# Optimization experiments

Hardware: AMD Instinct MI355X
Metric: run time of the kernel (lower is better)

The kernel has to match this reference:

```python
import jax, jax.numpy as jnp
import numpy as np

B, SEQ, DIM, D, K = 32, 2048, 512, 512, 128


def _ln(x, g, b, eps=1e-5):
    m = x.mean(-1, keepdims=True)
    v = ((x - m) ** 2).mean(-1, keepdims=True)
    return (x - m) / jnp.sqrt(v + eps) * g + b


def _gelu(v):
    return jax.nn.gelu(v, approximate=False)


def _diff_topk(s, k, t):
    # s: (B, N) scores; iterative relaxed top-k (Xie & Ermon style).
    def step(carry, _):
        a = jax.nn.softmax(carry / t, axis=-1)
        carry = carry + jnp.log(jnp.clip(1.0 - a, 1e-6, 1.0))
        return carry, a
    _, Ws = jax.lax.scan(step, s, None, length=k)  # (k, B, N)
    return jnp.transpose(Ws, (1, 0, 2))            # (B, k, N)


def setup_inputs():
    key = jax.random.key(0)
    ks = jax.random.split(key, 6)
    w = lambda k_, shape: jax.random.normal(k_, shape, dtype=jnp.float32) * 0.02
    return {
        'x': jax.random.normal(ks[0], (B, SEQ, DIM), dtype=jnp.float32),
        'tau': jnp.array(0.0, dtype=jnp.float32),
        'ln1_g': jnp.ones((DIM,), jnp.float32), 'ln1_b': jnp.zeros((DIM,), jnp.float32),
        'W1': w(ks[1], (DIM, D)), 'b1': jnp.zeros((D,), jnp.float32),
        'ln2_g': jnp.ones((SEQ,), jnp.float32), 'ln2_b': jnp.zeros((SEQ,), jnp.float32),
        'W2': w(ks[2], (SEQ, SEQ)), 'b2': jnp.zeros((SEQ,), jnp.float32),
        'ln3_g': jnp.ones((D,), jnp.float32), 'ln3_b': jnp.zeros((D,), jnp.float32),
        'W3': w(ks[3], (D, D + 1)), 'b3': jnp.zeros((D + 1,), jnp.float32),
        'ln4_g': jnp.ones((D,), jnp.float32), 'ln4_b': jnp.zeros((D,), jnp.float32),
        'W4': w(ks[4], (D, DIM)), 'b4': jnp.zeros((DIM,), jnp.float32),
    }


def reference(x, tau, ln1_g, ln1_b, W1, b1, ln2_g, ln2_b, W2, b2,
              ln3_g, ln3_b, W3, b3, ln4_g, ln4_b, W4, b4):
    # tok_proj: LN(dim) -> Linear(dim, D) -> GELU
    x_tok = _gelu(_ln(x, ln1_g, ln1_b) @ W1 + b1)                  # (B, N, D)
    # ch_proj over the token axis: LN(seq) -> Linear(seq, seq) -> GELU
    xt = jnp.swapaxes(x_tok, 1, 2)                                  # (B, D, N)
    x_ch = jnp.swapaxes(_gelu(_ln(xt, ln2_g, ln2_b) @ W2 + b2), 1, 2)
    # proj -> split score | features
    h = _ln(x_tok + x_ch, ln3_g, ln3_b) @ W3 + b3                   # (B, N, D+1)
    x_score, x_proj = h[..., 0], h[..., 1:]
    t = jax.nn.sigmoid(jnp.clip(tau, -2.0, 5.0))
    Wmat = _diff_topk(x_score, K, t)                                # (B, k, N)
    Z = jnp.einsum('bkn,bnd->bkd', Wmat, x_proj)                    # soft gather
    Y = jnp.einsum('bkn,bkd->bnd', Wmat, Z)                         # soft scatter
    return _ln(x_proj + Y, ln4_g, ln4_b) @ W4 + b4                  # (B, N, dim)
```

## Files before the change

kernel.cpp:

```cpp
#include <hip/hip_runtime.h>
#include <math.h>

#define B_   32
#define SEQ_ 2048
#define DIM_ 512
#define KSEL 128

typedef _Float16 f16;
typedef _Float16 half8 __attribute__((ext_vector_type(8)));
typedef float floatx4 __attribute__((ext_vector_type(4)));

#define LSTR2 32

__device__ __forceinline__ float gelu_exact(float v) {
  return 0.5f * v * (1.0f + erff(v * 0.70710678118654752440f));
}

__global__ __launch_bounds__(256) void rowstats512(const float* __restrict__ X,
                                                   float* __restrict__ mean,
                                                   float* __restrict__ rstd) {
  int row = blockIdx.x * 4 + (threadIdx.x >> 6);
  int l = threadIdx.x & 63;
  const float4* p = (const float4*)(X + (size_t)row * 512);
  float4 v0 = p[l * 2], v1 = p[l * 2 + 1];
  float s = v0.x + v0.y + v0.z + v0.w + v1.x + v1.y + v1.z + v1.w;
  float q = v0.x*v0.x + v0.y*v0.y + v0.z*v0.z + v0.w*v0.w
          + v1.x*v1.x + v1.y*v1.y + v1.z*v1.z + v1.w*v1.w;
#pragma unroll
  for (int off = 32; off > 0; off >>= 1) {
    s += __shfl_down(s, off);
    q += __shfl_down(q, off);
  }
  if (l == 0) {
    float m = s * (1.0f / 512.0f);
    float var = q * (1.0f / 512.0f) - m * m;
    mean[row] = m;
    rstd[row] = rsqrtf(var + 1e-5f);
  }
}

__global__ __launch_bounds__(256) void rowstats512_f16(const f16* __restrict__ X,
                                                       float* __restrict__ mean,
                                                       float* __restrict__ rstd) {
  int row = blockIdx.x * 4 + (threadIdx.x >> 6);
  int l = threadIdx.x & 63;
  half8 h = *(const half8*)(X + (size_t)row * 512 + l * 8);
  float s = 0.f, q = 0.f;
#pragma unroll
  for (int i = 0; i < 8; ++i) { float v = (float)h[i]; s += v; q += v * v; }
#pragma unroll
  for (int off = 32; off > 0; off >>= 1) {
    s += __shfl_down(s, off);
    q += __shfl_down(q, off);
  }
  if (l == 0) {
    float m = s * (1.0f / 512.0f);
    float var = q * (1.0f / 512.0f) - m * m;
    mean[row] = m;
    rstd[row] = rsqrtf(var + 1e-5f);
  }
}

__global__ __launch_bounds__(512) void colstats_part(const f16* __restrict__ xtok,
                                                     float2* __restrict__ part) {
  int b = blockIdx.x >> 3, pr = blockIdx.x & 7;
  int d = threadIdx.x;
  const f16* src = xtok + ((size_t)b * SEQ_ + (size_t)pr * 256) * 512 + d;
  float s = 0.f, q = 0.f;
#pragma unroll 4
  for (int i = 0; i < 256; ++i) {
    float v = (float)src[(size_t)i * 512];
    s += v; q += v * v;
  }
  part[(size_t)blockIdx.x * 512 + d] = make_float2(s, q);
}

__global__ __launch_bounds__(256) void colstats_fin(const float2* __restrict__ part,
                                                    float* __restrict__ mean,
                                                    float* __restrict__ rstd) {
  int idx = blockIdx.x * 256 + threadIdx.x;
  int b = idx >> 9;
  float s = 0.f, q = 0.f;
#pragma unroll
  for (int p = 0; p < 8; ++p) {
    float2 v = part[((size_t)(b * 8 + p)) * 512 + (idx & 511)];
    s += v.x; q += v.y;
  }
  float m = s * (1.0f / 2048.0f);
  mean[idx] = m;
  rstd[idx] = rsqrtf(q * (1.0f / 2048.0f) - m * m + 1e-5f);
}

template <typename T>
__global__ __launch_bounds__(256) void transpose_cvt(const T* __restrict__ src,
                                                     f16* __restrict__ dst,
                                                     int R, int C, long sb, long db) {
  __shared__ float tile[32][33];
  const T* s = src + (long)blockIdx.z * sb;
  f16* d = dst + (long)blockIdx.z * db;
  int c0 = blockIdx.x * 32, r0 = blockIdx.y * 32;
  int tx = threadIdx.x, ty = threadIdx.y;
#pragma unroll
  for (int i = 0; i < 4; ++i) {
    int r = r0 + ty + i * 8, c = c0 + tx;
    if (r < R && c < C) tile[ty + i * 8][tx] = (float)s[(long)r * C + c];
  }
  __syncthreads();
#pragma unroll
  for (int i = 0; i < 4; ++i) {
    int c = c0 + ty + i * 8, r = r0 + tx;
    if (c < C && r < R) d[(long)c * R + r] = (f16)tile[tx][ty + i * 8];
  }
}

__global__ __launch_bounds__(256) void trans2_kernel(const f16* __restrict__ xtok,
    const float* __restrict__ mean2, const float* __restrict__ rstd2,
    const float* __restrict__ g2, const float* __restrict__ bl2,
    f16* __restrict__ A2) {
  __shared__ float tile[32][33];
  int b = blockIdx.z;
  const f16* src = xtok + (long)b * SEQ_ * 512;
  f16* dst = A2 + (long)b * 512 * SEQ_;
  int d0 = blockIdx.x * 32, s0 = blockIdx.y * 32;
  int tx = threadIdx.x, ty = threadIdx.y;
  float m = mean2[b * 512 + d0 + tx];
  float rs = rstd2[b * 512 + d0 + tx];
#pragma unroll
  for (int i = 0; i < 4; ++i) {
    int s = s0 + ty + i * 8;
    float v = (float)src[(long)s * 512 + d0 + tx];
    tile[ty + i * 8][tx] = (v - m) * rs * g2[s] + bl2[s];
  }
  __syncthreads();
#pragma unroll
  for (int i = 0; i < 4; ++i) {
    int d = d0 + ty + i * 8, s = s0 + tx;
    dst[(long)d * SEQ_ + s] = (f16)tile[tx][ty + i * 8];
  }
}


__device__ __forceinline__ void stage_gll(const f16* __restrict__ src, long ld,
                                          int row0, int k0, f16* S, int t) {
  int w = t >> 6, lane = t & 63;
  int r = lane >> 2, c8 = (lane & 3) * 8;
#pragma unroll
  for (int i = 0; i < 2; ++i) {
    int chunk = w * 2 + i;
    const f16* g = src + (long)(row0 + chunk * 16 + r) * ld + k0 + c8;
    f16* l = S + chunk * 16 * LSTR2;
    __builtin_amdgcn_global_load_lds(
        (const __attribute__((address_space(1))) void*)g,
        (__attribute__((address_space(3))) void*)l, 16, 0, 0);
  }
}

__device__ __forceinline__ void stage_a_ln_f32(const float* __restrict__ src, long ld,
    const float* __restrict__ mean, const float* __restrict__ rstd,
    const float* __restrict__ g, const float* __restrict__ bl,
    int row0, int k0, f16* S, int t) {
  int row = t >> 1, kc = (t & 1) * 16;
  int r = row0 + row, c = k0 + kc;
  float m = mean[r], sd = rstd[r];
  const float* p = src + (long)r * ld + c;
  float v[16], gv[16], bv[16];
#pragma unroll
  for (int i = 0; i < 4; ++i) {
    float4 q = ((const float4*)p)[i];
    v[i*4+0]=q.x; v[i*4+1]=q.y; v[i*4+2]=q.z; v[i*4+3]=q.w;
    float4 gq = ((const float4*)(g + c))[i];
    gv[i*4+0]=gq.x; gv[i*4+1]=gq.y; gv[i*4+2]=gq.z; gv[i*4+3]=gq.w;
    float4 bq = ((const float4*)(bl + c))[i];
    bv[i*4+0]=bq.x; bv[i*4+1]=bq.y; bv[i*4+2]=bq.z; bv[i*4+3]=bq.w;
  }
  half8 o0, o1;
#pragma unroll
  for (int i = 0; i < 8; ++i) {
    o0[i] = (f16)((v[i] - m) * sd * gv[i] + bv[i]);
    o1[i] = (f16)((v[i + 8] - m) * sd * gv[i + 8] + bv[i + 8]);
  }
  *(half8*)(S + row * LSTR2 + kc) = o0;
  *(half8*)(S + row * LSTR2 + kc + 8) = o1;
}

__device__ __forceinline__ void stage_a_ln_f16(const f16* __restrict__ src, long ld,
    const float* __restrict__ mean, const float* __restrict__ rstd,
    const float* __restrict__ g, const float* __restrict__ bl,
    int row0, int k0, f16* S, int t) {
  int row = t >> 1, kc = (t & 1) * 16;
  int r = row0 + row, c = k0 + kc;
  float m = mean[r], sd = rstd[r];
  const f16* p = src + (long)r * ld + c;
  half8 h0 = *(const half8*)(p);
  half8 h1 = *(const half8*)(p + 8);
  float gv[16], bv[16];
#pragma unroll
  for (int i = 0; i < 4; ++i) {
    float4 gq = ((const float4*)(g + c))[i];
    gv[i*4+0]=gq.x; gv[i*4+1]=gq.y; gv[i*4+2]=gq.z; gv[i*4+3]=gq.w;
    float4 bq = ((const float4*)(bl + c))[i];
    bv[i*4+0]=bq.x; bv[i*4+1]=bq.y; bv[i*4+2]=bq.z; bv[i*4+3]=bq.w;
  }
  half8 o0, o1;
#pragma unroll
  for (int i = 0; i < 8; ++i) {
    o0[i] = (f16)(((float)h0[i] - m) * sd * gv[i] + bv[i]);
    o1[i] = (f16)(((float)h1[i] - m) * sd * gv[i + 8] + bv[i + 8]);
  }
  *(half8*)(S + row * LSTR2 + kc) = o0;
  *(half8*)(S + row * LSTR2 + kc + 8) = o1;
}

__device__ __forceinline__ void mfma_step(const f16* As, const f16* Bs, int lane,
                                          int wr, int wc, floatx4 acc[4][4]) {
  int kc = (lane >> 4) * 8;
  int rl = lane & 15;
  half8 a[4], b[4];
#pragma unroll
  for (int mi = 0; mi < 4; ++mi)
    a[mi] = *(const half8*)(As + (wr * 64 + mi * 16 + rl) * LSTR2 + kc);
#pragma unroll
  for (int ni = 0; ni < 4; ++ni)
    b[ni] = *(const half8*)(Bs + (wc * 64 + ni * 16 + rl) * LSTR2 + kc);
#pragma unroll
  for (int mi = 0; mi < 4; ++mi)
#pragma unroll
    for (int ni = 0; ni < 4; ++ni)
      acc[mi][ni] = __builtin_amdgcn_mfma_f32_16x16x32_f16(a[mi], b[ni], acc[mi][ni], 0, 0, 0);
}

#define GEMM_PROLOG \
  __shared__ __attribute__((aligned(16))) f16 As[128 * LSTR2]; \
  __shared__ __attribute__((aligned(16))) f16 Bs[128 * LSTR2]; \
  int t = threadIdx.x; \
  int lane = t & 63, w = t >> 6, wr = w >> 1, wc = w & 1; \
  floatx4 acc[4][4]; \
  _Pragma("unroll") for (int mi = 0; mi < 4; ++mi) \
  _Pragma("unroll") for (int ni = 0; ni < 4; ++ni) acc[mi][ni] = (floatx4){0.f,0.f,0.f,0.f};

__global__ __launch_bounds__(256) void g1_kernel(const float* __restrict__ x,
    const float* __restrict__ mean, const float* __restrict__ rstd,
    const float* __restrict__ g1, const float* __restrict__ bl1,
    const f16* __restrict__ W1T, const float* __restrict__ b1,
    f16* __restrict__ xtok) {
  GEMM_PROLOG
  int m0 = blockIdx.y * 128, n0 = blockIdx.x * 128;
  for (int k0 = 0; k0 < 512; k0 += 32) {
    stage_a_ln_f32(x, 512, mean, rstd, g1, bl1, m0, k0, As, t);
    stage_gll(W1T, 512, n0, k0, Bs, t);
    __syncthreads();
    mfma_step(As, Bs, lane, wr, wc, acc);
    __syncthreads();
  }
#pragma unroll
  for (int mi = 0; mi < 4; ++mi)
#pragma unroll
    for (int ni = 0; ni < 4; ++ni) {
      int c = n0 + wc * 64 + ni * 16 + (lane & 15);
      float bias = b1[c];
      int r0 = m0 + wr * 64 + mi * 16 + (lane >> 4) * 4;
#pragma unroll
      for (int j = 0; j < 4; ++j)
        xtok[(long)(r0 + j) * 512 + c] = (f16)gelu_exact(acc[mi][ni][j] + bias);
    }
}

__global__ __launch_bounds__(256) void g2_kernel(const f16* __restrict__ W2T,
    const f16* __restrict__ A2, const float* __restrict__ b2,
    const f16* __restrict__ xtok, f16* __restrict__ xsum) {
  GEMM_PROLOG
  int b = blockIdx.z;
  int m0 = blockIdx.y * 128, n0 = blockIdx.x * 128;
  const f16* A2b = A2 + (long)b * 512 * SEQ_;
  const f16* xtb = xtok + (long)b * SEQ_ * 512;
  f16* xsb = xsum + (long)b * SEQ_ * 512;
  for (int k0 = 0; k0 < SEQ_; k0 += 32) {
    stage_gll(W2T, SEQ_, m0, k0, As, t);
    stage_gll(A2b, SEQ_, n0, k0, Bs, t);
    __syncthreads();
    mfma_step(As, Bs, lane, wr, wc, acc);
    __syncthreads();
  }
#pragma unroll
  for (int mi = 0; mi < 4; ++mi)
#pragma unroll
    for (int ni = 0; ni < 4; ++ni) {
      int c = n0 + wc * 64 + ni * 16 + (lane & 15);
      int r0 = m0 + wr * 64 + mi * 16 + (lane >> 4) * 4;
#pragma unroll
      for (int j = 0; j < 4; ++j) {
        int r = r0 + j;
        long idx = (long)r * 512 + c;
        float v = gelu_exact(acc[mi][ni][j] + b2[r]);
        xsb[idx] = (f16)((float)xtb[idx] + v);
      }
    }
}

__global__ __launch_bounds__(256) void g3_kernel(const f16* __restrict__ xsum,
    const float* __restrict__ mean, const float* __restrict__ rstd,
    const float* __restrict__ g3, const float* __restrict__ bl3,
    const f16* __restrict__ BT , const float* __restrict__ b3,
    f16* __restrict__ xproj) {
  GEMM_PROLOG
  int m0 = blockIdx.y * 128, n0 = blockIdx.x * 128;
  for (int k0 = 0; k0 < 512; k0 += 32) {
    stage_a_ln_f16(xsum, 512, mean, rstd, g3, bl3, m0, k0, As, t);
    stage_gll(BT, 512, n0, k0, Bs, t);
    __syncthreads();
    mfma_step(As, Bs, lane, wr, wc, acc);
    __syncthreads();
  }
#pragma unroll
  for (int mi = 0; mi < 4; ++mi)
#pragma unroll
    for (int ni = 0; ni < 4; ++ni) {
      int c = n0 + wc * 64 + ni * 16 + (lane & 15);
      float bias = b3[c + 1];
      int r0 = m0 + wr * 64 + mi * 16 + (lane >> 4) * 4;
#pragma unroll
      for (int j = 0; j < 4; ++j)
        xproj[(long)(r0 + j) * 512 + c] = (f16)(acc[mi][ni][j] + bias);
    }
}

__global__ __launch_bounds__(256) void score_kernel(const f16* __restrict__ xsum,
    const float* __restrict__ mean, const float* __restrict__ rstd,
    const float* __restrict__ g3, const float* __restrict__ bl3,
    const f16* __restrict__ w3c , const float* __restrict__ b3,
    float* __restrict__ xscore) {
  int row = blockIdx.x * 4 + (threadIdx.x >> 6);
  int l = threadIdx.x & 63;
  float m = mean[row], sd = rstd[row];
  half8 h = *(const half8*)(xsum + (long)row * 512 + l * 8);
  half8 wv = *(const half8*)(w3c + l * 8);
  float acc = 0.f;
#pragma unroll
  for (int i = 0; i < 8; ++i) {
    int d = l * 8 + i;
    float v = ((float)h[i] - m) * sd * g3[d] + bl3[d];
    acc += v * (float)wv[i];
  }
#pragma unroll
  for (int off = 32; off > 0; off >>= 1) acc += __shfl_down(acc, off);
  if (l == 0) xscore[row] = acc + b3[0];
}

__global__ __launch_bounds__(256) void topk_kernel(const float* __restrict__ xscore,
                                                   const float* __restrict__ tau,
                                                   f16* __restrict__ Wm) {
  int b = blockIdx.x, t = threadIdx.x;
  __shared__ float red[4];
  float tv = fminf(fmaxf(tau[0], -2.0f), 5.0f);
  float temp = 1.0f / (1.0f + expf(-tv));
  float it = 1.0f / temp;
  float c[8];
  const float* xs = xscore + (size_t)b * SEQ_;
#pragma unroll
  for (int i = 0; i < 8; ++i) c[i] = xs[t * 8 + i];
  for (int k = 0; k < KSEL; ++k) {
    float e[8];
    float p = 0.f;
#pragma unroll
    for (int i = 0; i < 8; ++i) { e[i] = expf(c[i] * it); p += e[i]; }
#pragma unroll
    for (int off = 32; off > 0; off >>= 1) p += __shfl_down(p, off);
    if ((t & 63) == 0) red[t >> 6] = p;
    __syncthreads();
    float S = red[0] + red[1] + red[2] + red[3];
    float iS = 1.0f / S;
    float a[8];
    half8 h;
#pragma unroll
    for (int i = 0; i < 8; ++i) { a[i] = e[i] * iS; h[i] = (f16)a[i]; }
    *(half8*)(Wm + ((size_t)b * KSEL + k) * SEQ_ + t * 8) = h;
#pragma unroll
    for (int i = 0; i < 8; ++i) c[i] += logf(fmaxf(1.0f - a[i], 1e-6f));
    __syncthreads();
  }
}

__global__ __launch_bounds__(256) void gz_kernel(const f16* __restrict__ Wm,
    const f16* __restrict__ xprojT, float* __restrict__ Zpart) {
  GEMM_PROLOG
  int b = blockIdx.z, kc = blockIdx.y;
  int n0 = blockIdx.x * 128;
  const f16* A = Wm + (long)b * KSEL * SEQ_;
  const f16* BT = xprojT + (long)b * 512 * SEQ_;
  float* Zb = Zpart + ((long)b * 2 + kc) * KSEL * 512;
  int kbeg = kc * 1024, kend = kbeg + 1024;
  for (int k0 = kbeg; k0 < kend; k0 += 32) {
    stage_gll(A, SEQ_, 0, k0, As, t);
    stage_gll(BT, SEQ_, n0, k0, Bs, t);
    __syncthreads();
    mfma_step(As, Bs, lane, wr, wc, acc);
    __syncthreads();
  }
#pragma unroll
  for (int mi = 0; mi < 4; ++mi)
#pragma unroll
    for (int ni = 0; ni < 4; ++ni) {
      int c = n0 + wc * 64 + ni * 16 + (lane & 15);
      int r0 = wr * 64 + mi * 16 + (lane >> 4) * 4;
#pragma unroll
      for (int j = 0; j < 4; ++j)
        Zb[(long)(r0 + j) * 512 + c] = acc[mi][ni][j];
    }
}

__global__ __launch_bounds__(256) void ztrans_kernel(const float* __restrict__ Zpart,
                                                     f16* __restrict__ ZT) {
  __shared__ float tile[32][33];
  int b = blockIdx.z;
  int c0 = blockIdx.x * 32, r0 = blockIdx.y * 32;
  int tx = threadIdx.x, ty = threadIdx.y;
  const float* p0 = Zpart + ((long)b * 2 + 0) * KSEL * 512;
  const float* p1 = Zpart + ((long)b * 2 + 1) * KSEL * 512;
#pragma unroll
  for (int i = 0; i < 4; ++i) {
    int r = r0 + ty + i * 8, c = c0 + tx;
    tile[ty + i * 8][tx] = p0[(long)r * 512 + c] + p1[(long)r * 512 + c];
  }
  __syncthreads();
  f16* d = ZT + (long)b * 512 * KSEL;
#pragma unroll
  for (int i = 0; i < 4; ++i) {
    int c = c0 + ty + i * 8, r = r0 + tx;
    d[(long)c * KSEL + r] = (f16)tile[tx][ty + i * 8];
  }
}

__global__ __launch_bounds__(256) void gy_kernel(const f16* __restrict__ WmT,
    const f16* __restrict__ ZT, const f16* __restrict__ xproj,
    f16* __restrict__ rbuf) {
  GEMM_PROLOG
  int b = blockIdx.z;
  int m0 = blockIdx.y * 128, n0 = blockIdx.x * 128;
  const f16* A = WmT + (long)b * SEQ_ * KSEL;
  const f16* BT = ZT + (long)b * 512 * KSEL;
  const f16* xpb = xproj + (long)b * SEQ_ * 512;
  f16* rb = rbuf + (long)b * SEQ_ * 512;
  for (int k0 = 0; k0 < KSEL; k0 += 32) {
    stage_gll(A, KSEL, m0, k0, As, t);
    stage_gll(BT, KSEL, n0, k0, Bs, t);
    __syncthreads();
    mfma_step(As, Bs, lane, wr, wc, acc);
    __syncthreads();
  }
#pragma unroll
  for (int mi = 0; mi < 4; ++mi)
#pragma unroll
    for (int ni = 0; ni < 4; ++ni) {
      int c = n0 + wc * 64 + ni * 16 + (lane & 15);
      int r0 = m0 + wr * 64 + mi * 16 + (lane >> 4) * 4;
#pragma unroll
      for (int j = 0; j < 4; ++j) {
        long idx = (long)(r0 + j) * 512 + c;
        rb[idx] = (f16)((float)xpb[idx] + acc[mi][ni][j]);
      }
    }
}

__global__ __launch_bounds__(256) void g4_kernel(const f16* __restrict__ rbuf,
    const float* __restrict__ mean, const float* __restrict__ rstd,
    const float* __restrict__ g4, const float* __restrict__ bl4,
    const f16* __restrict__ W4T, const float* __restrict__ b4,
    float* __restrict__ out) {
  GEMM_PROLOG
  int m0 = blockIdx.y * 128, n0 = blockIdx.x * 128;
  for (int k0 = 0; k0 < 512; k0 += 32) {
    stage_a_ln_f16(rbuf, 512, mean, rstd, g4, bl4, m0, k0, As, t);
    stage_gll(W4T, 512, n0, k0, Bs, t);
    __syncthreads();
    mfma_step(As, Bs, lane, wr, wc, acc);
    __syncthreads();
  }
#pragma unroll
  for (int mi = 0; mi < 4; ++mi)
#pragma unroll
    for (int ni = 0; ni < 4; ++ni) {
      int c = n0 + wc * 64 + ni * 16 + (lane & 15);
      float bias = b4[c];
      int r0 = m0 + wr * 64 + mi * 16 + (lane >> 4) * 4;
#pragma unroll
      for (int j = 0; j < 4; ++j)
        out[(long)(r0 + j) * 512 + c] = acc[mi][ni][j] + bias;
    }
}

extern "C" void kernel_launch(void* const* d_in, const int* in_sizes, int n_in,
                              void* d_out, int out_size, void* d_ws, size_t ws_size,
                              hipStream_t stream) {
  const float* x    = (const float*)d_in[0];
  const float* tau  = (const float*)d_in[1];
  const float* g1   = (const float*)d_in[2];
  const float* bl1  = (const float*)d_in[3];
  const float* W1   = (const float*)d_in[4];
  const float* b1   = (const float*)d_in[5];
  const float* g2   = (const float*)d_in[6];
  const float* bl2  = (const float*)d_in[7];
  const float* W2   = (const float*)d_in[8];
  const float* b2   = (const float*)d_in[9];
  const float* g3   = (const float*)d_in[10];
  const float* bl3  = (const float*)d_in[11];
  const float* W3   = (const float*)d_in[12];
  const float* b3   = (const float*)d_in[13];
  const float* g4   = (const float*)d_in[14];
  const float* bl4  = (const float*)d_in[15];
  const float* W4   = (const float*)d_in[16];
  const float* b4   = (const float*)d_in[17];
  float* out = (float*)d_out;

  const long NTOK = (long)B_ * SEQ_;

  char* ws = (char*)d_ws;
  f16* regA   = (f16*)(ws);
  f16* regB   = (f16*)(ws + (64l << 20));
  float* Zpart = (float*)(ws + (128l << 20));
  f16* W2T    = (f16*)(ws + (144l << 20));
  f16* W1T    = (f16*)(ws + (152l << 20));
  f16* W3T    = (f16*)(ws + (153l << 20));
  f16* W4T    = (f16*)(ws + (154l << 20));
  float* xscore = (float*)(ws + (155l << 20));
  float* meanA  = (float*)(ws + (156l << 20));
  float* rstdA  = meanA + NTOK;
  float* mean2  = rstdA + NTOK;
  float* rstd2  = mean2 + B_ * 512;
  float2* part  = (float2*)(rstd2 + B_ * 512);

  f16* xtok   = (f16*)d_out;
  f16* xprojT = (f16*)d_out;
  f16* Wm     = (f16*)((char*)d_out + (64l << 20));
  f16* WmT    = (f16*)((char*)d_out + (80l << 20));
  f16* ZT     = (f16*)((char*)d_out + (96l << 20));

  f16* A2    = regA;
  f16* xsum  = regB;
  f16* xproj = regA;
  f16* rbuf  = regB;

  dim3 tb(32, 8);

  transpose_cvt<float><<<dim3(16, 16, 1), tb, 0, stream>>>(W1, W1T, 512, 512, 0, 0);
  transpose_cvt<float><<<dim3(64, 64, 1), tb, 0, stream>>>(W2, W2T, 2048, 2048, 0, 0);
  transpose_cvt<float><<<dim3(17, 16, 1), tb, 0, stream>>>(W3, W3T, 512, 513, 0, 0);
  transpose_cvt<float><<<dim3(16, 16, 1), tb, 0, stream>>>(W4, W4T, 512, 512, 0, 0);

  rowstats512<<<NTOK / 4, 256, 0, stream>>>(x, meanA, rstdA);
  g1_kernel<<<dim3(4, 512), 256, 0, stream>>>(x, meanA, rstdA, g1, bl1, W1T, b1, xtok);

  colstats_part<<<B_ * 8, 512, 0, stream>>>(xtok, part);
  colstats_fin<<<64, 256, 0, stream>>>(part, mean2, rstd2);
  trans2_kernel<<<dim3(16, 64, B_), tb, 0, stream>>>(xtok, mean2, rstd2, g2, bl2, A2);
  g2_kernel<<<dim3(4, 16, B_), 256, 0, stream>>>(W2T, A2, b2, xtok, xsum);

  rowstats512_f16<<<NTOK / 4, 256, 0, stream>>>(xsum, meanA, rstdA);
  score_kernel<<<NTOK / 4, 256, 0, stream>>>(xsum, meanA, rstdA, g3, bl3, W3T, b3, xscore);
  g3_kernel<<<dim3(4, 512), 256, 0, stream>>>(xsum, meanA, rstdA, g3, bl3, W3T + 512, b3, xproj);

  topk_kernel<<<B_, 256, 0, stream>>>(xscore, tau, Wm);

  transpose_cvt<f16><<<dim3(16, 64, B_), tb, 0, stream>>>(xproj, xprojT, 2048, 512,
      (long)SEQ_ * 512, (long)512 * SEQ_);
  transpose_cvt<f16><<<dim3(64, 4, B_), tb, 0, stream>>>(Wm, WmT, 128, 2048,
      (long)KSEL * SEQ_, (long)SEQ_ * KSEL);

  gz_kernel<<<dim3(4, 2, B_), 256, 0, stream>>>(Wm, xprojT, Zpart);
  ztrans_kernel<<<dim3(16, 4, B_), tb, 0, stream>>>(Zpart, ZT);

  gy_kernel<<<dim3(4, 16, B_), 256, 0, stream>>>(WmT, ZT, xproj, rbuf);

  rowstats512_f16<<<NTOK / 4, 256, 0, stream>>>(rbuf, meanA, rstdA);
  g4_kernel<<<dim3(4, 512), 256, 0, stream>>>(rbuf, meanA, rstdA, g4, bl4, W4T, b4, out);
}
```

Measured before the change: 878.3 us.

## Double-buffer GEMMs with 64-wide swizzled K tiles, fuse xproj transpose, widen topk

All MFMA GEMM kernels now stage 64-wide K tiles into double-buffered, XOR-swizzled LDS. The next tile is prefetched while the current one is computed, with one barrier per step and s_setprio raised around the MFMAs. The aim is to overlap global loads with compute and to cut LDS bank conflicts. g3 also writes a transposed copy of xproj directly, which removes a separate transpose pass. topk runs with 512 threads and one barrier per iteration using ping-pong reduction slots. The larger LDS footprint may lower occupancy.

```diff
diff --git a/kernel.cpp b/kernel.cpp
--- a/kernel.cpp
+++ b/kernel.cpp
@@ -8,9 +8,8 @@
 
 typedef _Float16 f16;
 typedef _Float16 half8 __attribute__((ext_vector_type(8)));
+typedef _Float16 half4 __attribute__((ext_vector_type(4)));
 typedef float floatx4 __attribute__((ext_vector_type(4)));
-
-#define LSTR2 32
 
 __device__ __forceinline__ float gelu_exact(float v) {
   return 0.5f * v * (1.0f + erff(v * 0.70710678118654752440f));
@@ -140,100 +139,123 @@
 }
 
 
-__device__ __forceinline__ void stage_gll(const f16* __restrict__ src, long ld,
-                                          int row0, int k0, f16* S, int t) {
-  int w = t >> 6, lane = t & 63;
-  int r = lane >> 2, c8 = (lane & 3) * 8;
-#pragma unroll
-  for (int i = 0; i < 2; ++i) {
-    int chunk = w * 2 + i;
-    const f16* g = src + (long)(row0 + chunk * 16 + r) * ld + k0 + c8;
-    f16* l = S + chunk * 16 * LSTR2;
-    __builtin_amdgcn_global_load_lds(
-        (const __attribute__((address_space(1))) void*)g,
-        (__attribute__((address_space(3))) void*)l, 16, 0, 0);
-  }
-}
-
-__device__ __forceinline__ void stage_a_ln_f32(const float* __restrict__ src, long ld,
+__device__ __forceinline__ void stage_tile_gll(const f16* __restrict__ src, long ld,
+                                               int k0, f16* D0, f16* D1, int t) {
+  int w = t >> 6;
+#pragma unroll
+  for (int kk = 0; kk < 2; ++kk) {
+    f16* dst = kk ? D1 : D0;
+#pragma unroll
+    for (int s = 0; s < 2; ++s) {
+      int row = s * 64 + (t >> 2);
+      int slot = (t & 3) ^ ((row >> 1) & 3);
+      const f16* g = src + (long)row * ld + k0 + kk * 32 + slot * 8;
+      f16* lp = dst + (long)(s * 64 + w * 16) * 32;
+      __builtin_amdgcn_global_load_lds(
+          (const __attribute__((address_space(1))) void*)g,
+          (__attribute__((address_space(3))) void*)lp, 16, 0, 0);
+    }
+  }
+}
+
+__device__ __forceinline__ void stage_a_ln_f32_64(const float* __restrict__ src, long ld,
     const float* __restrict__ mean, const float* __restrict__ rstd,
     const float* __restrict__ g, const float* __restrict__ bl,
-    int row0, int k0, f16* S, int t) {
-  int row = t >> 1, kc = (t & 1) * 16;
-  int r = row0 + row, c = k0 + kc;
+    int row0, int k0, f16* D0, f16* D1, int t) {
+  int row = t >> 1, kk = t & 1;
+  int r = row0 + row;
   float m = mean[r], sd = rstd[r];
-  const float* p = src + (long)r * ld + c;
-  float v[16], gv[16], bv[16];
-#pragma unroll
-  for (int i = 0; i < 4; ++i) {
-    float4 q = ((const float4*)p)[i];
-    v[i*4+0]=q.x; v[i*4+1]=q.y; v[i*4+2]=q.z; v[i*4+3]=q.w;
-    float4 gq = ((const float4*)(g + c))[i];
-    gv[i*4+0]=gq.x; gv[i*4+1]=gq.y; gv[i*4+2]=gq.z; gv[i*4+3]=gq.w;
-    float4 bq = ((const float4*)(bl + c))[i];
-    bv[i*4+0]=bq.x; bv[i*4+1]=bq.y; bv[i*4+2]=bq.z; bv[i*4+3]=bq.w;
-  }
-  half8 o0, o1;
-#pragma unroll
-  for (int i = 0; i < 8; ++i) {
-    o0[i] = (f16)((v[i] - m) * sd * gv[i] + bv[i]);
-    o1[i] = (f16)((v[i + 8] - m) * sd * gv[i + 8] + bv[i + 8]);
-  }
-  *(half8*)(S + row * LSTR2 + kc) = o0;
-  *(half8*)(S + row * LSTR2 + kc + 8) = o1;
-}
-
-__device__ __forceinline__ void stage_a_ln_f16(const f16* __restrict__ src, long ld,
+  f16* dst = (kk ? D1 : D0) + row * 32;
+  int swz = (row >> 1) & 3;
+  const float* p = src + (long)r * ld + k0 + kk * 32;
+  const float* gp = g + k0 + kk * 32;
+  const float* bp = bl + k0 + kk * 32;
+#pragma unroll
+  for (int j = 0; j < 4; ++j) {
+    float4 q0 = *(const float4*)(p + j * 8);
+    float4 q1 = *(const float4*)(p + j * 8 + 4);
+    float4 g0 = *(const float4*)(gp + j * 8);
+    float4 g1 = *(const float4*)(gp + j * 8 + 4);
+    float4 b0 = *(const float4*)(bp + j * 8);
+    float4 b1 = *(const float4*)(bp + j * 8 + 4);
+    half8 o;
+    o[0] = (f16)((q0.x - m) * sd * g0.x + b0.x);
+    o[1] = (f16)((q0.y - m) * sd * g0.y + b0.y);
+    o[2] = (f16)((q0.z - m) * sd * g0.z + b0.z);
+    o[3] = (f16)((q0.w - m) * sd * g0.w + b0.w);
+    o[4] = (f16)((q1.x - m) * sd * g1.x + b1.x);
+    o[5] = (f16)((q1.y - m) * sd * g1.y + b1.y);
+    o[6] = (f16)((q1.z - m) * sd * g1.z + b1.z);
+    o[7] = (f16)((q1.w - m) * sd * g1.w + b1.w);
+    *(half8*)(dst + ((j ^ swz) << 3)) = o;
+  }
+}
+
+__device__ __forceinline__ void stage_a_ln_f16_64(const f16* __restrict__ src, long ld,
     const float* __restrict__ mean, const float* __restrict__ rstd,
     const float* __restrict__ g, const float* __restrict__ bl,
-    int row0, int k0, f16* S, int t) {
-  int row = t >> 1, kc = (t & 1) * 16;
-  int r = row0 + row, c = k0 + kc;
+    int row0, int k0, f16* D0, f16* D1, int t) {
+  int row = t >> 1, kk = t & 1;
+  int r = row0 + row;
   float m = mean[r], sd = rstd[r];
-  const f16* p = src + (long)r * ld + c;
-  half8 h0 = *(const half8*)(p);
-  half8 h1 = *(const half8*)(p + 8);
-  float gv[16], bv[16];
-#pragma unroll
-  for (int i = 0; i < 4; ++i) {
-    float4 gq = ((const float4*)(g + c))[i];
-    gv[i*4+0]=gq.x; gv[i*4+1]=gq.y; gv[i*4+2]=gq.z; gv[i*4+3]=gq.w;
-    float4 bq = ((const float4*)(bl + c))[i];
-    bv[i*4+0]=bq.x; bv[i*4+1]=bq.y; bv[i*4+2]=bq.z; bv[i*4+3]=bq.w;
-  }
-  half8 o0, o1;
-#pragma unroll
-  for (int i = 0; i < 8; ++i) {
-    o0[i] = (f16)(((float)h0[i] - m) * sd * gv[i] + bv[i]);
-    o1[i] = (f16)(((float)h1[i] - m) * sd * gv[i + 8] + bv[i + 8]);
-  }
-  *(half8*)(S + row * LSTR2 + kc) = o0;
-  *(half8*)(S + row * LSTR2 + kc + 8) = o1;
-}
-
-__device__ __forceinline__ void mfma_step(const f16* As, const f16* Bs, int lane,
-                                          int wr, int wc, floatx4 acc[4][4]) {
-  int kc = (lane >> 4) * 8;
-  int rl = lane & 15;
-  half8 a[4], b[4];
-#pragma unroll
-  for (int mi = 0; mi < 4; ++mi)
-    a[mi] = *(const half8*)(As + (wr * 64 + mi * 16 + rl) * LSTR2 + kc);
-#pragma unroll
-  for (int ni = 0; ni < 4; ++ni)
-    b[ni] = *(const half8*)(Bs + (wc * 64 + ni * 16 + rl) * LSTR2 + kc);
-#pragma unroll
-  for (int mi = 0; mi < 4; ++mi)
-#pragma unroll
-    for (int ni = 0; ni < 4; ++ni)
-      acc[mi][ni] = __builtin_amdgcn_mfma_f32_16x16x32_f16(a[mi], b[ni], acc[mi][ni], 0, 0, 0);
-}
-
-#define GEMM_PROLOG \
-  __shared__ __attribute__((aligned(16))) f16 As[128 * LSTR2]; \
-  __shared__ __attribute__((aligned(16))) f16 Bs[128 * LSTR2]; \
+  f16* dst = (kk ? D1 : D0) + row * 32;
+  int swz = (row >> 1) & 3;
+  const f16* p = src + (long)r * ld + k0 + kk * 32;
+  const float* gp = g + k0 + kk * 32;
+  const float* bp = bl + k0 + kk * 32;
+#pragma unroll
+  for (int j = 0; j < 4; ++j) {
+    half8 h = *(const half8*)(p + j * 8);
+    float4 g0 = *(const float4*)(gp + j * 8);
+    float4 g1 = *(const float4*)(gp + j * 8 + 4);
+    float4 b0 = *(const float4*)(bp + j * 8);
+    float4 b1 = *(const float4*)(bp + j * 8 + 4);
+    half8 o;
+    o[0] = (f16)(((float)h[0] - m) * sd * g0.x + b0.x);
+    o[1] = (f16)(((float)h[1] - m) * sd * g0.y + b0.y);
+    o[2] = (f16)(((float)h[2] - m) * sd * g0.z + b0.z);
+    o[3] = (f16)(((float)h[3] - m) * sd * g0.w + b0.w);
+    o[4] = (f16)(((float)h[4] - m) * sd * g1.x + b1.x);
+    o[5] = (f16)(((float)h[5] - m) * sd * g1.y + b1.y);
+    o[6] = (f16)(((float)h[6] - m) * sd * g1.z + b1.z);
+    o[7] = (f16)(((float)h[7] - m) * sd * g1.w + b1.w);
+    *(half8*)(dst + ((j ^ swz) << 3)) = o;
+  }
+}
+
+__device__ __forceinline__ half8 frag32(const f16* buf, int row, int sl) {
+  return *(const half8*)(buf + (long)row * 32 + ((sl ^ ((row >> 1) & 3)) << 3));
+}
+
+__device__ __forceinline__ void tile_mfma(const f16* A0, const f16* A1,
+                                          const f16* B0, const f16* B1,
+                                          int wr, int wc, int rl, int sl,
+                                          floatx4 acc[4][4]) {
+  half8 afr[4], bfr[4];
+#pragma unroll
+  for (int kk = 0; kk < 2; ++kk) {
+    const f16* Ab = kk ? A1 : A0;
+    const f16* Bb = kk ? B1 : B0;
+#pragma unroll
+    for (int mi = 0; mi < 4; ++mi) afr[mi] = frag32(Ab, wr * 64 + mi * 16 + rl, sl);
+#pragma unroll
+    for (int ni = 0; ni < 4; ++ni) bfr[ni] = frag32(Bb, wc * 64 + ni * 16 + rl, sl);
+    __builtin_amdgcn_s_setprio(1);
+#pragma unroll
+    for (int mi = 0; mi < 4; ++mi)
+#pragma unroll
+      for (int ni = 0; ni < 4; ++ni)
+        acc[mi][ni] = __builtin_amdgcn_mfma_f32_16x16x32_f16(afr[mi], bfr[ni], acc[mi][ni], 0, 0, 0);
+    __builtin_amdgcn_s_setprio(0);
+  }
+}
+
+#define ENGINE_PROLOG \
+  __shared__ __attribute__((aligned(16))) f16 Ah[2][2][128 * 32]; \
+  __shared__ __attribute__((aligned(16))) f16 Bh[2][2][128 * 32]; \
   int t = threadIdx.x; \
   int lane = t & 63, w = t >> 6, wr = w >> 1, wc = w & 1; \
+  int rl = lane & 15, sl = lane >> 4; \
   floatx4 acc[4][4]; \
   _Pragma("unroll") for (int mi = 0; mi < 4; ++mi) \
   _Pragma("unroll") for (int ni = 0; ni < 4; ++ni) acc[mi][ni] = (floatx4){0.f,0.f,0.f,0.f};
@@ -243,54 +265,69 @@
     const float* __restrict__ g1, const float* __restrict__ bl1,
     const f16* __restrict__ W1T, const float* __restrict__ b1,
     f16* __restrict__ xtok) {
-  GEMM_PROLOG
+  ENGINE_PROLOG
   int m0 = blockIdx.y * 128, n0 = blockIdx.x * 128;
-  for (int k0 = 0; k0 < 512; k0 += 32) {
-    stage_a_ln_f32(x, 512, mean, rstd, g1, bl1, m0, k0, As, t);
-    stage_gll(W1T, 512, n0, k0, Bs, t);
+  const int NT = 512 / 64;
+  stage_a_ln_f32_64(x, 512, mean, rstd, g1, bl1, m0, 0, Ah[0][0], Ah[0][1], t);
+  stage_tile_gll(W1T + (long)n0 * 512, 512, 0, Bh[0][0], Bh[0][1], t);
+  __syncthreads();
+  for (int kt = 0; kt < NT; ++kt) {
+    int c = kt & 1;
+    if (kt + 1 < NT) {
+      stage_a_ln_f32_64(x, 512, mean, rstd, g1, bl1, m0, (kt + 1) * 64,
+                        Ah[c ^ 1][0], Ah[c ^ 1][1], t);
+      stage_tile_gll(W1T + (long)n0 * 512, 512, (kt + 1) * 64,
+                     Bh[c ^ 1][0], Bh[c ^ 1][1], t);
+    }
+    tile_mfma(Ah[c][0], Ah[c][1], Bh[c][0], Bh[c][1], wr, wc, rl, sl, acc);
     __syncthreads();
-    mfma_step(As, Bs, lane, wr, wc, acc);
-    __syncthreads();
   }
 #pragma unroll
   for (int mi = 0; mi < 4; ++mi)
 #pragma unroll
     for (int ni = 0; ni < 4; ++ni) {
-      int c = n0 + wc * 64 + ni * 16 + (lane & 15);
-      float bias = b1[c];
-      int r0 = m0 + wr * 64 + mi * 16 + (lane >> 4) * 4;
+      int cc = n0 + wc * 64 + ni * 16 + rl;
+      float bias = b1[cc];
+      int r0 = m0 + wr * 64 + mi * 16 + sl * 4;
 #pragma unroll
       for (int j = 0; j < 4; ++j)
-        xtok[(long)(r0 + j) * 512 + c] = (f16)gelu_exact(acc[mi][ni][j] + bias);
+        xtok[(long)(r0 + j) * 512 + cc] = (f16)gelu_exact(acc[mi][ni][j] + bias);
     }
 }
 
 __global__ __launch_bounds__(256) void g2_kernel(const f16* __restrict__ W2T,
     const f16* __restrict__ A2, const float* __restrict__ b2,
     const f16* __restrict__ xtok, f16* __restrict__ xsum) {
-  GEMM_PROLOG
+  ENGINE_PROLOG
   int b = blockIdx.z;
   int m0 = blockIdx.y * 128, n0 = blockIdx.x * 128;
-  const f16* A2b = A2 + (long)b * 512 * SEQ_;
+  const f16* Am = W2T + (long)m0 * SEQ_;
+  const f16* Bm = A2 + (long)b * 512 * SEQ_ + (long)n0 * SEQ_;
   const f16* xtb = xtok + (long)b * SEQ_ * 512;
   f16* xsb = xsum + (long)b * SEQ_ * 512;
-  for (int k0 = 0; k0 < SEQ_; k0 += 32) {
-    stage_gll(W2T, SEQ_, m0, k0, As, t);
-    stage_gll(A2b, SEQ_, n0, k0, Bs, t);
+  const int NT = SEQ_ / 64;
+  stage_tile_gll(Am, SEQ_, 0, Ah[0][0], Ah[0][1], t);
+  stage_tile_gll(Bm, SEQ_, 0, Bh[0][0], Bh[0][1], t);
+  __syncthreads();
+  for (int kt = 0; kt < NT; ++kt) {
+    int c = kt & 1;
+    if (kt + 1 < NT) {
+      stage_tile_gll(Am, SEQ_, (kt + 1) * 64, Ah[c ^ 1][0], Ah[c ^ 1][1], t);
+      stage_tile_gll(Bm, SEQ_, (kt + 1) * 64, Bh[c ^ 1][0], Bh[c ^ 1][1], t);
+    }
+    tile_mfma(Ah[c][0], Ah[c][1], Bh[c][0], Bh[c][1], wr, wc, rl, sl, acc);
     __syncthreads();
-    mfma_step(As, Bs, lane, wr, wc, acc);
-    __syncthreads();
   }
 #pragma unroll
   for (int mi = 0; mi < 4; ++mi)
 #pragma unroll
     for (int ni = 0; ni < 4; ++ni) {
-      int c = n0 + wc * 64 + ni * 16 + (lane & 15);
-      int r0 = m0 + wr * 64 + mi * 16 + (lane >> 4) * 4;
+      int cc = n0 + wc * 64 + ni * 16 + rl;
+      int r0 = m0 + wr * 64 + mi * 16 + sl * 4;
 #pragma unroll
       for (int j = 0; j < 4; ++j) {
         int r = r0 + j;
-        long idx = (long)r * 512 + c;
+        long idx = (long)r * 512 + cc;
         float v = gelu_exact(acc[mi][ni][j] + b2[r]);
         xsb[idx] = (f16)((float)xtb[idx] + v);
       }
@@ -301,33 +338,48 @@
     const float* __restrict__ mean, const float* __restrict__ rstd,
     const float* __restrict__ g3, const float* __restrict__ bl3,
     const f16* __restrict__ BT , const float* __restrict__ b3,
-    f16* __restrict__ xproj) {
-  GEMM_PROLOG
+    f16* __restrict__ xproj, f16* __restrict__ xprojT) {
+  ENGINE_PROLOG
   int m0 = blockIdx.y * 128, n0 = blockIdx.x * 128;
-  for (int k0 = 0; k0 < 512; k0 += 32) {
-    stage_a_ln_f16(xsum, 512, mean, rstd, g3, bl3, m0, k0, As, t);
-    stage_gll(BT, 512, n0, k0, Bs, t);
+  const int NT = 512 / 64;
+  stage_a_ln_f16_64(xsum, 512, mean, rstd, g3, bl3, m0, 0, Ah[0][0], Ah[0][1], t);
+  stage_tile_gll(BT + (long)n0 * 512, 512, 0, Bh[0][0], Bh[0][1], t);
+  __syncthreads();
+  for (int kt = 0; kt < NT; ++kt) {
+    int c = kt & 1;
+    if (kt + 1 < NT) {
+      stage_a_ln_f16_64(xsum, 512, mean, rstd, g3, bl3, m0, (kt + 1) * 64,
+                        Ah[c ^ 1][0], Ah[c ^ 1][1], t);
+      stage_tile_gll(BT + (long)n0 * 512, 512, (kt + 1) * 64,
+                     Bh[c ^ 1][0], Bh[c ^ 1][1], t);
+    }
+    tile_mfma(Ah[c][0], Ah[c][1], Bh[c][0], Bh[c][1], wr, wc, rl, sl, acc);
     __syncthreads();
-    mfma_step(As, Bs, lane, wr, wc, acc);
-    __syncthreads();
   }
 #pragma unroll
   for (int mi = 0; mi < 4; ++mi)
 #pragma unroll
     for (int ni = 0; ni < 4; ++ni) {
-      int c = n0 + wc * 64 + ni * 16 + (lane & 15);
-      float bias = b3[c + 1];
-      int r0 = m0 + wr * 64 + mi * 16 + (lane >> 4) * 4;
-#pragma unroll
-      for (int j = 0; j < 4; ++j)
-        xproj[(long)(r0 + j) * 512 + c] = (f16)(acc[mi][ni][j] + bias);
+      int cc = n0 + wc * 64 + ni * 16 + rl;
+      float bias = b3[cc + 1];
+      int r0 = m0 + wr * 64 + mi * 16 + sl * 4;
+      half4 xp;
+#pragma unroll
+      for (int j = 0; j < 4; ++j) {
+        f16 v = (f16)(acc[mi][ni][j] + bias);
+        xproj[(long)(r0 + j) * 512 + cc] = v;
+        xp[j] = v;
+      }
+      long bb = r0 >> 11;
+      long rloc = r0 & 2047;
+      *(half4*)(xprojT + (bb * 512 + cc) * SEQ_ + rloc) = xp;
     }
 }
 
 __global__ __launch_bounds__(256) void score_kernel(const f16* __restrict__ xsum,
     const float* __restrict__ mean, const float* __restrict__ rstd,
     const float* __restrict__ g3, const float* __restrict__ bl3,
-    const f16* __restrict__ w3c , const float* __restrict__ b3,
+    const f16* __restrict__ w3c, const float* __restrict__ b3,
     float* __restrict__ xscore) {
   int row = blockIdx.x * 4 + (threadIdx.x >> 6);
   int l = threadIdx.x & 63;
@@ -346,65 +398,75 @@
   if (l == 0) xscore[row] = acc + b3[0];
 }
 
-__global__ __launch_bounds__(256) void topk_kernel(const float* __restrict__ xscore,
+__global__ __launch_bounds__(512) void topk_kernel(const float* __restrict__ xscore,
                                                    const float* __restrict__ tau,
                                                    f16* __restrict__ Wm) {
   int b = blockIdx.x, t = threadIdx.x;
-  __shared__ float red[4];
+  __shared__ float red[2][8];
   float tv = fminf(fmaxf(tau[0], -2.0f), 5.0f);
   float temp = 1.0f / (1.0f + expf(-tv));
   float it = 1.0f / temp;
-  float c[8];
+  float c[4];
   const float* xs = xscore + (size_t)b * SEQ_;
-#pragma unroll
-  for (int i = 0; i < 8; ++i) c[i] = xs[t * 8 + i];
+  {
+    float4 v = *(const float4*)(xs + t * 4);
+    c[0] = v.x; c[1] = v.y; c[2] = v.z; c[3] = v.w;
+  }
+  int l = t & 63, wid = t >> 6;
   for (int k = 0; k < KSEL; ++k) {
-    float e[8];
+    float e[4];
     float p = 0.f;
 #pragma unroll
-    for (int i = 0; i < 8; ++i) { e[i] = expf(c[i] * it); p += e[i]; }
+    for (int i = 0; i < 4; ++i) { e[i] = expf(c[i] * it); p += e[i]; }
 #pragma unroll
     for (int off = 32; off > 0; off >>= 1) p += __shfl_down(p, off);
-    if ((t & 63) == 0) red[t >> 6] = p;
+    if (l == 0) red[k & 1][wid] = p;
     __syncthreads();
-    float S = red[0] + red[1] + red[2] + red[3];
+    float S = 0.f;
+#pragma unroll
+    for (int q = 0; q < 8; ++q) S += red[k & 1][q];
     float iS = 1.0f / S;
-    float a[8];
-    half8 h;
-#pragma unroll
-    for (int i = 0; i < 8; ++i) { a[i] = e[i] * iS; h[i] = (f16)a[i]; }
-    *(half8*)(Wm + ((size_t)b * KSEL + k) * SEQ_ + t * 8) = h;
-#pragma unroll
-    for (int i = 0; i < 8; ++i) c[i] += logf(fmaxf(1.0f - a[i], 1e-6f));
-    __syncthreads();
+    half4 h;
+    float a[4];
+#pragma unroll
+    for (int i = 0; i < 4; ++i) { a[i] = e[i] * iS; h[i] = (f16)a[i]; }
+    *(half4*)(Wm + ((size_t)b * KSEL + k) * SEQ_ + t * 4) = h;
+#pragma unroll
+    for (int i = 0; i < 4; ++i) c[i] += logf(fmaxf(1.0f - a[i], 1e-6f));
   }
 }
 
 __global__ __launch_bounds__(256) void gz_kernel(const f16* __restrict__ Wm,
     const f16* __restrict__ xprojT, float* __restrict__ Zpart) {
-  GEMM_PROLOG
+  ENGINE_PROLOG
   int b = blockIdx.z, kc = blockIdx.y;
   int n0 = blockIdx.x * 128;
-  const f16* A = Wm + (long)b * KSEL * SEQ_;
-  const f16* BT = xprojT + (long)b * 512 * SEQ_;
+  const f16* Am = Wm + (long)b * KSEL * SEQ_;
+  const f16* Bm = xprojT + (long)b * 512 * SEQ_ + (long)n0 * SEQ_;
   float* Zb = Zpart + ((long)b * 2 + kc) * KSEL * 512;
-  int kbeg = kc * 1024, kend = kbeg + 1024;
-  for (int k0 = kbeg; k0 < kend; k0 += 32) {
-    stage_gll(A, SEQ_, 0, k0, As, t);
-    stage_gll(BT, SEQ_, n0, k0, Bs, t);
+  int kbeg = kc * 1024;
+  const int NT = 1024 / 64;
+  stage_tile_gll(Am, SEQ_, kbeg, Ah[0][0], Ah[0][1], t);
+  stage_tile_gll(Bm, SEQ_, kbeg, Bh[0][0], Bh[0][1], t);
+  __syncthreads();
+  for (int kt = 0; kt < NT; ++kt) {
+    int c = kt & 1;
+    if (kt + 1 < NT) {
+      stage_tile_gll(Am, SEQ_, kbeg + (kt + 1) * 64, Ah[c ^ 1][0], Ah[c ^ 1][1], t);
+      stage_tile_gll(Bm, SEQ_, kbeg + (kt + 1) * 64, Bh[c ^ 1][0], Bh[c ^ 1][1], t);
+    }
+    tile_mfma(Ah[c][0], Ah[c][1], Bh[c][0], Bh[c][1], wr, wc, rl, sl, acc);
     __syncthreads();
-    mfma_step(As, Bs, lane, wr, wc, acc);
-    __syncthreads();
   }
 #pragma unroll
   for (int mi = 0; mi < 4; ++mi)
 #pragma unroll
     for (int ni = 0; ni < 4; ++ni) {
-      int c = n0 + wc * 64 + ni * 16 + (lane & 15);
-      int r0 = wr * 64 + mi * 16 + (lane >> 4) * 4;
+      int cc = n0 + wc * 64 + ni * 16 + rl;
+      int r0 = wr * 64 + mi * 16 + sl * 4;
 #pragma unroll
       for (int j = 0; j < 4; ++j)
-        Zb[(long)(r0 + j) * 512 + c] = acc[mi][ni][j];
+        Zb[(long)(r0 + j) * 512 + cc] = acc[mi][ni][j];
     }
 }
 
@@ -433,29 +495,35 @@
 __global__ __launch_bounds__(256) void gy_kernel(const f16* __restrict__ WmT,
     const f16* __restrict__ ZT, const f16* __restrict__ xproj,
     f16* __restrict__ rbuf) {
-  GEMM_PROLOG
+  ENGINE_PROLOG
   int b = blockIdx.z;
   int m0 = blockIdx.y * 128, n0 = blockIdx.x * 128;
-  const f16* A = WmT + (long)b * SEQ_ * KSEL;
-  const f16* BT = ZT + (long)b * 512 * KSEL;
+  const f16* Am = WmT + (long)b * SEQ_ * KSEL + (long)m0 * KSEL;
+  const f16* Bm = ZT + (long)b * 512 * KSEL + (long)n0 * KSEL;
   const f16* xpb = xproj + (long)b * SEQ_ * 512;
   f16* rb = rbuf + (long)b * SEQ_ * 512;
-  for (int k0 = 0; k0 < KSEL; k0 += 32) {
-    stage_gll(A, KSEL, m0, k0, As, t);
-    stage_gll(BT, KSEL, n0, k0, Bs, t);
+  const int NT = KSEL / 64;
+  stage_tile_gll(Am, KSEL, 0, Ah[0][0], Ah[0][1], t);
+  stage_tile_gll(Bm, KSEL, 0, Bh[0][0], Bh[0][1], t);
+  __syncthreads();
+  for (int kt = 0; kt < NT; ++kt) {
+    int c = kt & 1;
+    if (kt + 1 < NT) {
+      stage_tile_gll(Am, KSEL, (kt + 1) * 64, Ah[c ^ 1][0], Ah[c ^ 1][1], t);
+      stage_tile_gll(Bm, KSEL, (kt + 1) * 64, Bh[c ^ 1][0], Bh[c ^ 1][1], t);
+    }
+    tile_mfma(Ah[c][0], Ah[c][1], Bh[c][0], Bh[c][1], wr, wc, rl, sl, acc);
     __syncthreads();
-    mfma_step(As, Bs, lane, wr, wc, acc);
-    __syncthreads();
   }
 #pragma unroll
   for (int mi = 0; mi < 4; ++mi)
 #pragma unroll
     for (int ni = 0; ni < 4; ++ni) {
-      int c = n0 + wc * 64 + ni * 16 + (lane & 15);
-      int r0 = m0 + wr * 64 + mi * 16 + (lane >> 4) * 4;
+      int cc = n0 + wc * 64 + ni * 16 + rl;
+      int r0 = m0 + wr * 64 + mi * 16 + sl * 4;
 #pragma unroll
       for (int j = 0; j < 4; ++j) {
-        long idx = (long)(r0 + j) * 512 + c;
+        long idx = (long)(r0 + j) * 512 + cc;
         rb[idx] = (f16)((float)xpb[idx] + acc[mi][ni][j]);
       }
     }
@@ -466,25 +534,33 @@
     const float* __restrict__ g4, const float* __restrict__ bl4,
     const f16* __restrict__ W4T, const float* __restrict__ b4,
     float* __restrict__ out) {
-  GEMM_PROLOG
+  ENGINE_PROLOG
   int m0 = blockIdx.y * 128, n0 = blockIdx.x * 128;
-  for (int k0 = 0; k0 < 512; k0 += 32) {
-    stage_a_ln_f16(rbuf, 512, mean, rstd, g4, bl4, m0, k0, As, t);
-    stage_gll(W4T, 512, n0, k0, Bs, t);
+  const int NT = 512 / 64;
+  stage_a_ln_f16_64(rbuf, 512, mean, rstd, g4, bl4, m0, 0, Ah[0][0], Ah[0][1], t);
+  stage_tile_gll(W4T + (long)n0 * 512, 512, 0, Bh[0][0], Bh[0][1], t);
+  __syncthreads();
+  for (int kt = 0; kt < NT; ++kt) {
+    int c = kt & 1;
+    if (kt + 1 < NT) {
+      stage_a_ln_f16_64(rbuf, 512, mean, rstd, g4, bl4, m0, (kt + 1) * 64,
+                        Ah[c ^ 1][0], Ah[c ^ 1][1], t);
+      stage_tile_gll(W4T + (long)n0 * 512, 512, (kt + 1) * 64,
+                     Bh[c ^ 1][0], Bh[c ^ 1][1], t);
+    }
+    tile_mfma(Ah[c][0], Ah[c][1], Bh[c][0], Bh[c][1], wr, wc, rl, sl, acc);
     __syncthreads();
-    mfma_step(As, Bs, lane, wr, wc, acc);
-    __syncthreads();
   }
 #pragma unroll
   for (int mi = 0; mi < 4; ++mi)
 #pragma unroll
     for (int ni = 0; ni < 4; ++ni) {
-      int c = n0 + wc * 64 + ni * 16 + (lane & 15);
-      float bias = b4[c];
-      int r0 = m0 + wr * 64 + mi * 16 + (lane >> 4) * 4;
+      int cc = n0 + wc * 64 + ni * 16 + rl;
+      float bias = b4[cc];
+      int r0 = m0 + wr * 64 + mi * 16 + sl * 4;
 #pragma unroll
       for (int j = 0; j < 4; ++j)
-        out[(long)(r0 + j) * 512 + c] = acc[mi][ni][j] + bias;
+        out[(long)(r0 + j) * 512 + cc] = acc[mi][ni][j] + bias;
     }
 }
 
@@ -527,12 +603,12 @@
   float* mean2  = rstdA + NTOK;
   float* rstd2  = mean2 + B_ * 512;
   float2* part  = (float2*)(rstd2 + B_ * 512);
+  f16* ZT     = (f16*)(ws + (157l << 20));
 
   f16* xtok   = (f16*)d_out;
   f16* xprojT = (f16*)d_out;
   f16* Wm     = (f16*)((char*)d_out + (64l << 20));
   f16* WmT    = (f16*)((char*)d_out + (80l << 20));
-  f16* ZT     = (f16*)((char*)d_out + (96l << 20));
 
   f16* A2    = regA;
   f16* xsum  = regB;
@@ -556,12 +632,11 @@
 
   rowstats512_f16<<<NTOK / 4, 256, 0, stream>>>(xsum, meanA, rstdA);
   score_kernel<<<NTOK / 4, 256, 0, stream>>>(xsum, meanA, rstdA, g3, bl3, W3T, b3, xscore);
-  g3_kernel<<<dim3(4, 512), 256, 0, stream>>>(xsum, meanA, rstdA, g3, bl3, W3T + 512, b3, xproj);
-
-  topk_kernel<<<B_, 256, 0, stream>>>(xscore, tau, Wm);
-
-  transpose_cvt<f16><<<dim3(16, 64, B_), tb, 0, stream>>>(xproj, xprojT, 2048, 512,
-      (long)SEQ_ * 512, (long)512 * SEQ_);
+  g3_kernel<<<dim3(4, 512), 256, 0, stream>>>(xsum, meanA, rstdA, g3, bl3, W3T + 512, b3,
+                                              xproj, xprojT);
+
+  topk_kernel<<<B_, 512, 0, stream>>>(xscore, tau, Wm);
+
   transpose_cvt<f16><<<dim3(64, 4, B_), tb, 0, stream>>>(Wm, WmT, 128, 2048,
       (long)KSEL * SEQ_, (long)SEQ_ * KSEL);
 
```

After: 965.5 us. 1.1x slower.
